# Performance work log

Measured on AMD Instinct MI355X. Metric: run time of the kernel, lower is better.

## Reference

```python
import jax, jax.numpy as jnp
import numpy as np

B, C, T = 32, 64, 1024        # batch_size, in_channels, cycle_size
H, D = 2, 64                  # GATv2 heads, per-head dim (dim_h)
DIM2 = H * D                  # dim_h * 2 = 128
K = 9                         # temporal_kernel_size
N = B * T                     # graph nodes after flatten
E = 524288                    # edges (avg degree 16)
EPS = 1e-5


def bn3d(x, gamma, beta):
    # BatchNorm1d on [B, C, T] in training mode (batch statistics)
    mu = x.mean(axis=(0, 2), keepdims=True)
    var = x.var(axis=(0, 2), keepdims=True)
    xn = (x - mu) * jax.lax.rsqrt(var + EPS)
    return xn * gamma[None, :, None] + beta[None, :, None]


def bn2d(x, gamma, beta):
    # BatchNorm1d on [N, C] in training mode
    mu = x.mean(axis=0, keepdims=True)
    var = x.var(axis=0, keepdims=True)
    return (x - mu) * jax.lax.rsqrt(var + EPS) * gamma + beta


def conv1d_same(x, w, b):
    # x: [B, Cin, T], w: [Cout, Cin, K]
    y = jax.lax.conv_general_dilated(x, w, (1,), 'SAME',
                                     dimension_numbers=('NCH', 'OIH', 'NCH'))
    return y + b[None, :, None]


def gatv2(x, edge_index, wl, wr, att, bias):
    # PyG GATv2Conv defaults: heads=H, concat=True, leaky slope 0.2, self-loops
    loops = jnp.arange(N, dtype=edge_index.dtype)
    src = jnp.concatenate([edge_index[0], loops])
    dst = jnp.concatenate([edge_index[1], loops])
    xl = (x @ wl.T).reshape(N, H, D)   # source transform
    xr = (x @ wr.T).reshape(N, H, D)   # target transform
    m = jax.nn.leaky_relu(xl[src] + xr[dst], 0.2)        # [E+N, H, D]
    logits = jnp.einsum('ehd,hd->eh', m, att)            # [E+N, H]
    lmax = jax.ops.segment_max(logits, dst, num_segments=N)
    lmax = jax.lax.stop_gradient(jnp.where(jnp.isfinite(lmax), lmax, 0.0))
    p = jnp.exp(logits - lmax[dst])
    denom = jax.ops.segment_sum(p, dst, num_segments=N)  # >0: self-loops
    alpha = p / denom[dst]                               # softmax over in-edges
    out = jax.ops.segment_sum(xl[src] * alpha[:, :, None], dst, num_segments=N)
    return out.reshape(N, DIM2) + bias


def setup_inputs() -> dict:
    key = jax.random.key(0)
    ks = jax.random.split(key, 10)
    s = lambda k, shape: jax.random.normal(k, shape, jnp.float32) * 0.05
    return {
        'x': jax.random.normal(ks[0], (B, C, T), jnp.float32),
        'edge_index': jax.random.randint(ks[1], (2, E), 0, N, jnp.int32),
        'bn0_gamma': jnp.ones((C,), jnp.float32),
        'bn0_beta': jnp.zeros((C,), jnp.float32),
        'conv_w': s(ks[2], (DIM2, C, K)),
        'conv_b': s(ks[3], (DIM2,)),
        'gat_wl': s(ks[4], (DIM2, C)),
        'gat_wr': s(ks[5], (DIM2, C)),
        'gat_att': s(ks[6], (H, D)),
        'gat_bias': s(ks[7], (DIM2,)),
        'bn1_gamma': jnp.ones((DIM2,), jnp.float32),
        'bn1_beta': jnp.zeros((DIM2,), jnp.float32),
        'cheb_w': s(ks[8], (DIM2, DIM2)),
        'cheb_b': s(ks[9], (DIM2,)),
        'train': 0,
    }


def reference(x, edge_index, bn0_gamma, bn0_beta, conv_w, conv_b,
              gat_wl, gat_wr, gat_att, gat_bias, bn1_gamma, bn1_beta,
              cheb_w, cheb_b, train):
    x = bn3d(x, bn0_gamma, bn0_beta)                       # b0 (batch_size > 1)
    residual = jax.nn.relu(conv1d_same(x, conv_w, conv_b)) # skip_connection
    h = x.reshape(T * B, C)                                # flatten to nodes
    h = gatv2(h, edge_index, gat_wl, gat_wr, gat_att, gat_bias)
    h = jax.nn.relu(bn2d(h, bn1_gamma, bn1_beta))          # b1
    h = h.reshape(B, DIM2, T)
    h = residual + h
    # chain of views: (T*B,d) -> (B,d,T) -> (B,T,-1) -> (T*B,d); pure reshapes
    h = h.reshape(T * B, DIM2)
    h = h @ cheb_w.T + cheb_b                              # ChebConv K=1 == linear
    h = jax.nn.relu(bn2d(h, bn1_gamma, bn1_beta))          # b1 again
    h = h.reshape(B, DIM2, T)
    return residual + h                                    # dropout: identity (eval)
```

## Files before the change

kernel.cpp:

```cpp
#include <hip/hip_runtime.h>

#define DEVINL __device__ __forceinline__

constexpr int Bc = 32, Cc = 64, Tc = 1024, DIM2c = 128;
constexpr int Nn = Bc * Tc;
constexpr int Ec = 524288;

typedef __bf16 bf16x8 __attribute__((ext_vector_type(8)));
typedef __bf16 bf16x4 __attribute__((ext_vector_type(4)));
typedef float  f32x4  __attribute__((ext_vector_type(4)));

constexpr long O_RES   = 0;
constexpr long O_GOUT  = 4194304;
constexpr long O_XT    = 8388608;
constexpr long O_HBF   = 9437184;
constexpr long O_XLQ   = 10485760;
constexpr long O_XRQ   = 12582912;
constexpr long O_H2BF  = 14680064;
constexpr long O_Z     = 16777216;
constexpr long O_WCBF  = 20971520;
constexpr long O_WLR   = 21008384;
constexpr long O_CHB   = 21016576;
constexpr long O_STAT  = 21024768;
constexpr long O_CUR   = 21025792;
constexpr long O_BUCK  = 21058560;

DEVINL float unpack_lo(unsigned v) { return __uint_as_float(v << 16); }
DEVINL float unpack_hi(unsigned v) { return __uint_as_float(v & 0xffff0000u); }
DEVINL unsigned bfb(float f) { return (__float_as_uint(f) + 0x8000u) >> 16; }

__global__ __launch_bounds__(256) void setup(const float* __restrict__ x,
        const float* __restrict__ cw, const float* __restrict__ wl,
        const float* __restrict__ wr, const float* __restrict__ chw,
        const int* __restrict__ ei,
        __bf16* __restrict__ wcbf, __bf16* __restrict__ wlrbf,
        __bf16* __restrict__ chwbf,
        float* __restrict__ sum0, float* __restrict__ sq0,
        int* __restrict__ cursor, int* __restrict__ bucket) {
    int bid = blockIdx.x, tid = threadIdx.x;
    if (bid < 416) {
        int i = bid * 256 + tid;
        if (i < 73728) {
            int kk = i >> 13, co = (i >> 6) & 127, ci = i & 63;
            wcbf[i] = (__bf16)cw[co * 576 + ci * 9 + kk];
        } else if (i < 73728 + 16384) {
            int j = i - 73728;
            int r = j >> 6, c = j & 63;
            float v = (r < 128) ? wl[r * 64 + c] : wr[(r - 128) * 64 + c];
            wlrbf[j] = (__bf16)v;
        } else {
            int j = i - 73728 - 16384;
            chwbf[j] = (__bf16)chw[j];
        }
    } else if (bid < 672) {
        int pq = bid - 416;
        int c = pq & 63, q = pq >> 6;
        const float4* base = (const float4*)(x + (long)q * 8 * 65536 + (long)c * 1024);
        float s = 0.f, qq = 0.f;
        for (int i = tid; i < 2048; i += 256) {
            int b = i >> 8, t4 = i & 255;
            float4 v = base[b * 16384 + t4];
            s += v.x + v.y + v.z + v.w;
            qq = fmaf(v.x, v.x, qq); qq = fmaf(v.y, v.y, qq);
            qq = fmaf(v.z, v.z, qq); qq = fmaf(v.w, v.w, qq);
        }
        for (int off = 32; off; off >>= 1) { s += __shfl_down(s, off); qq += __shfl_down(qq, off); }
        __shared__ float ls[4], lq[4];
        int w = tid >> 6, lane = tid & 63;
        if (lane == 0) { ls[w] = s; lq[w] = qq; }
        __syncthreads();
        if (tid == 0) {
            unsafeAtomicAdd(sum0 + c, ls[0] + ls[1] + ls[2] + ls[3]);
            unsafeAtomicAdd(sq0 + c, lq[0] + lq[1] + lq[2] + lq[3]);
        }
    } else {
        int e = (bid - 672) * 256 + tid;
        int t = ei[Ec + e];
        int slot = atomicAdd(cursor + t, 1);
        bucket[t * 64 + slot] = ei[e];
    }
}

__global__ __launch_bounds__(256) void xprep(const float* __restrict__ x,
        const float* __restrict__ sum0, const float* __restrict__ sq0,
        const float* __restrict__ g0, const float* __restrict__ b0,
        __bf16* __restrict__ hbf, __bf16* __restrict__ xt) {
    __shared__ float lds[64][65];
    __shared__ float scs[64], shs[64];
    int tid = threadIdx.x;
    if (tid < 64) {
        float mu = sum0[tid] * (1.f / 32768.f);
        float var = sq0[tid] * (1.f / 32768.f) - mu * mu;
        float rs = rsqrtf(var + 1e-5f);
        float sc = rs * g0[tid];
        scs[tid] = sc; shs[tid] = b0[tid] - mu * sc;
    }
    __syncthreads();
    int t0 = blockIdx.x * 64;
    int b  = blockIdx.y;
    const float* xb = x + (long)b * 65536;
    for (int i = tid; i < 4096; i += 256) {
        int ci = i >> 6, tl = i & 63;
        float v = fmaf(xb[ci * 1024 + t0 + tl], scs[ci], shs[ci]);
        hbf[(long)b * 65536 + ci * 1024 + t0 + tl] = (__bf16)v;
        lds[ci][tl] = v;
    }
    __syncthreads();
    for (int i = tid; i < 4096; i += 256) {
        int t = i >> 6, ci = i & 63;
        xt[((long)b * 1024 + t0 + t) * 64 + ci] = (__bf16)lds[ci][t];
    }
}

constexpr int XS_STRIDE = 68;

DEVINL void conv_role(int cid, const __bf16* __restrict__ xt,
        const __bf16* __restrict__ wcbf, const float* __restrict__ cb,
        float* __restrict__ res, __bf16* xs) {
    int tid = threadIdx.x;
    int tbase = (cid & 7) * 128;
    int cohalf = (cid >> 3) & 1;
    int b = cid >> 4;
    const uint2* xg = (const uint2*)(xt + (long)b * 65536);
    for (int i = tid; i < 136 * 16; i += 256) {
        int row = i >> 4, c4 = i & 15;
        int t = tbase + row - 4;
        uint2 v; v.x = 0u; v.y = 0u;
        if ((unsigned)t < 1024u) v = xg[t * 16 + c4];
        *(uint2*)(xs + row * XS_STRIDE + c4 * 4) = v;
    }
    __syncthreads();
    int wv = tid >> 6, lane = tid & 63;
    int col = lane & 15, q = lane >> 4;
    int co0 = cohalf * 64 + wv * 16;
    bf16x8 af[18];
    #pragma unroll
    for (int kk = 0; kk < 9; kk++)
        #pragma unroll
        for (int ks = 0; ks < 2; ks++)
            af[kk * 2 + ks] = *(const bf16x8*)(wcbf +
                ((long)kk * 8192 + (long)(co0 + col) * 64 + ks * 32 + q * 8));
    float bi0 = cb[co0 + q * 4], bi1 = cb[co0 + q * 4 + 1];
    float bi2 = cb[co0 + q * 4 + 2], bi3 = cb[co0 + q * 4 + 3];
    for (int nt = 0; nt < 8; nt++) {
        int t0 = tbase + nt * 16;
        f32x4 acc; acc[0] = bi0; acc[1] = bi1; acc[2] = bi2; acc[3] = bi3;
        #pragma unroll
        for (int kk = 0; kk < 9; kk++) {
            const __bf16* rp = xs + (nt * 16 + col + kk) * XS_STRIDE + q * 8;
            #pragma unroll
            for (int ks = 0; ks < 2; ks++) {
                bf16x4 lo = *(const bf16x4*)(rp + ks * 32);
                bf16x4 hi = *(const bf16x4*)(rp + ks * 32 + 4);
                bf16x8 bfx;
                bfx[0]=lo[0]; bfx[1]=lo[1]; bfx[2]=lo[2]; bfx[3]=lo[3];
                bfx[4]=hi[0]; bfx[5]=hi[1]; bfx[6]=hi[2]; bfx[7]=hi[3];
                acc = __builtin_amdgcn_mfma_f32_16x16x32_bf16(af[kk * 2 + ks], bfx, acc, 0, 0, 0);
            }
        }
        long ob = (long)b * 131072 + (long)(co0 + q * 4) * 1024 + t0 + col;
        res[ob]        = fmaxf(acc[0], 0.f);
        res[ob + 1024] = fmaxf(acc[1], 0.f);
        res[ob + 2048] = fmaxf(acc[2], 0.f);
        res[ob + 3072] = fmaxf(acc[3], 0.f);
    }
}

DEVINL void gemm1_role(int mb, const __bf16* __restrict__ hbf,
        const __bf16* __restrict__ wlrbf,
        unsigned short* __restrict__ xl16, unsigned short* __restrict__ xr16) {
    int wv = threadIdx.x >> 6, lane = threadIdx.x & 63;
    int col = lane & 15, q = lane >> 4;
    int d0 = wv * 16;
    long mbase = (long)mb * 64;
    bf16x8 bfr[4][2];
    #pragma unroll
    for (int t = 0; t < 4; t++) {
        int j = d0 + t * 64 + col;
        #pragma unroll
        for (int ks = 0; ks < 2; ks++)
            bfr[t][ks] = *(const bf16x8*)(wlrbf + (long)j * 64 + ks * 32 + q * 8);
    }
    int d = d0 + col;
    for (int mt = 0; mt < 4; mt++) {
        long r0 = mbase + mt * 16;
        bf16x8 a0 = *(const bf16x8*)(hbf + (r0 + col) * 64 + q * 8);
        bf16x8 a1 = *(const bf16x8*)(hbf + (r0 + col) * 64 + 32 + q * 8);
        f32x4 acc[4];
        #pragma unroll
        for (int t = 0; t < 4; t++) { acc[t][0] = 0.f; acc[t][1] = 0.f; acc[t][2] = 0.f; acc[t][3] = 0.f; }
        #pragma unroll
        for (int t = 0; t < 4; t++) {
            acc[t] = __builtin_amdgcn_mfma_f32_16x16x32_bf16(a0, bfr[t][0], acc[t], 0, 0, 0);
            acc[t] = __builtin_amdgcn_mfma_f32_16x16x32_bf16(a1, bfr[t][1], acc[t], 0, 0, 0);
        }
        #pragma unroll
        for (int reg = 0; reg < 4; reg++) {
            long rb = (r0 + q * 4 + reg) * 128;
            xl16[rb + d]      = (unsigned short)bfb(acc[0][reg]);
            xl16[rb + 64 + d] = (unsigned short)bfb(acc[1][reg]);
            xr16[rb + d]      = (unsigned short)bfb(acc[2][reg]);
            xr16[rb + 64 + d] = (unsigned short)bfb(acc[3][reg]);
        }
    }
}

__global__ __launch_bounds__(256) void conv_gemm1(const __bf16* __restrict__ xt,
        const __bf16* __restrict__ wcbf, const float* __restrict__ cb,
        float* __restrict__ res, const __bf16* __restrict__ hbf,
        const __bf16* __restrict__ wlrbf,
        unsigned* __restrict__ xlq, unsigned* __restrict__ xrq) {
    __shared__ __bf16 xs[136 * XS_STRIDE];
    int bid = blockIdx.x;
    if (bid & 1) gemm1_role(bid >> 1, hbf, wlrbf, (unsigned short*)xlq, (unsigned short*)xrq);
    else conv_role(bid >> 1, xt, wcbf, cb, res, xs);
}

#define GAT_EDGE(VREG) {                                              \
    float xl_lo = unpack_lo(VREG), xl_hi = unpack_hi(VREG);           \
    float v0 = xl_lo + xr_lo; v0 = fmaxf(v0, 0.2f * v0);              \
    float v1 = xl_hi + xr_hi; v1 = fmaxf(v1, 0.2f * v1);              \
    float w2 = fmaf(v1, a_hi, v0 * a_lo);                             \
    _Pragma("unroll")                                                 \
    for (int off = 16; off; off >>= 1) w2 += __shfl_xor(w2, off);     \
    float e2 = __expf(w2);                                            \
    den += e2;                                                        \
    acc_lo = fmaf(e2, xl_lo, acc_lo);                                 \
    acc_hi = fmaf(e2, xl_hi, acc_hi);                                 \
}

__global__ __launch_bounds__(256) void gat_agg(const unsigned* __restrict__ xlq,
        const unsigned* __restrict__ xrq,
        const int* __restrict__ cursor, const int* __restrict__ bucket,
        const float* __restrict__ att, float* __restrict__ gout) {
    int wid = (blockIdx.x * 256 + threadIdx.x) >> 6;
    int lane = threadIdx.x & 63;
    int h = lane >> 5, dd = (lane & 31) * 2;
    float a_lo = att[h * 64 + dd], a_hi = att[h * 64 + dd + 1];
    int cnt = cursor[wid];
    int s_all = bucket[wid * 64 + lane];
    unsigned vr = xrq[(long)wid * 64 + lane];
    float xr_lo = unpack_lo(vr), xr_hi = unpack_hi(vr);
    unsigned vs = xlq[(long)wid * 64 + lane];
    float xs_lo = unpack_lo(vs), xs_hi = unpack_hi(vs);
    float u0 = xs_lo + xr_lo; u0 = fmaxf(u0, 0.2f * u0);
    float u1 = xs_hi + xr_hi; u1 = fmaxf(u1, 0.2f * u1);
    float w = fmaf(u1, a_hi, u0 * a_lo);
    #pragma unroll
    for (int off = 16; off; off >>= 1) w += __shfl_xor(w, off);
    float e = __expf(w);
    float den = e, acc_lo = e * xs_lo, acc_hi = e * xs_hi;
    unsigned pf0 = 0, pf1 = 0, pf2 = 0, pf3 = 0;
    {
        int s0 = __shfl(s_all, 0), s1 = __shfl(s_all, 1);
        int s2 = __shfl(s_all, 2), s3 = __shfl(s_all, 3);
        if (0 < cnt) pf0 = xlq[(long)s0 * 64 + lane];
        if (1 < cnt) pf1 = xlq[(long)s1 * 64 + lane];
        if (2 < cnt) pf2 = xlq[(long)s2 * 64 + lane];
        if (3 < cnt) pf3 = xlq[(long)s3 * 64 + lane];
    }
    int i = 0;
    for (; i + 4 <= cnt; i += 4) {
        unsigned v0 = pf0, v1 = pf1, v2 = pf2, v3 = pf3;
        int s4 = __shfl(s_all, i + 4), s5 = __shfl(s_all, i + 5);
        int s6 = __shfl(s_all, i + 6), s7 = __shfl(s_all, i + 7);
        if (i + 4 < cnt) pf0 = xlq[(long)s4 * 64 + lane];
        if (i + 5 < cnt) pf1 = xlq[(long)s5 * 64 + lane];
        if (i + 6 < cnt) pf2 = xlq[(long)s6 * 64 + lane];
        if (i + 7 < cnt) pf3 = xlq[(long)s7 * 64 + lane];
        GAT_EDGE(v0) GAT_EDGE(v1) GAT_EDGE(v2) GAT_EDGE(v3)
    }
    if (i < cnt) { GAT_EDGE(pf0) i++;
        if (i < cnt) { GAT_EDGE(pf1) i++;
            if (i < cnt) { GAT_EDGE(pf2) } } }
    float rn = __builtin_amdgcn_rcpf(den);
    float2 o; o.x = acc_lo * rn; o.y = acc_hi * rn;
    *(float2*)(gout + (long)wid * 128 + h * 64 + dd) = o;
}

__global__ __launch_bounds__(256) void bn_stats(const float* __restrict__ X,
        float* __restrict__ sum, float* __restrict__ sq) {
    int f = threadIdx.x & 127, sub = threadIdx.x >> 7;
    int r0 = blockIdx.x * 256;
    float s = 0.f, q = 0.f;
    for (int r = r0 + sub; r < r0 + 256; r += 2) {
        float v = X[(long)r * 128 + f];
        s += v; q = fmaf(v, v, q);
    }
    __shared__ float ls[256], lq[256];
    ls[threadIdx.x] = s; lq[threadIdx.x] = q;
    __syncthreads();
    if (threadIdx.x < 128) {
        s = ls[threadIdx.x] + ls[threadIdx.x + 128];
        q = lq[threadIdx.x] + lq[threadIdx.x + 128];
        unsafeAtomicAdd(sum + f, s);
        unsafeAtomicAdd(sq + f, q);
    }
}

__global__ __launch_bounds__(256) void bn_res_bf(const float* __restrict__ X,
        const float* __restrict__ res, const float* __restrict__ sum,
        const float* __restrict__ sq, const float* __restrict__ g,
        const float* __restrict__ bta, unsigned* __restrict__ outb) {
    __shared__ float scs[128], shs[128];
    int tid = threadIdx.x;
    if (tid < 128) {
        float mu = sum[tid] * (1.f / 32768.f);
        float var = sq[tid] * (1.f / 32768.f) - mu * mu;
        float rs = rsqrtf(var + 1e-5f);
        float sc = rs * g[tid];
        scs[tid] = sc; shs[tid] = bta[tid] - mu * sc;
    }
    __syncthreads();
    int idx = blockIdx.x * 256 + tid;
    int f0 = (idx & 31) * 4;
    float4 v = ((const float4*)X)[idx];
    float4 r = ((const float4*)res)[idx];
    float o0 = r.x + fmaxf(fmaf(v.x, scs[f0],     shs[f0]),     0.f);
    float o1 = r.y + fmaxf(fmaf(v.y, scs[f0 + 1], shs[f0 + 1]), 0.f);
    float o2 = r.z + fmaxf(fmaf(v.z, scs[f0 + 2], shs[f0 + 2]), 0.f);
    float o3 = r.w + fmaxf(fmaf(v.w, scs[f0 + 3], shs[f0 + 3]), 0.f);
    uint2 o; o.x = (bfb(o1) << 16) | bfb(o0); o.y = (bfb(o3) << 16) | bfb(o2);
    ((uint2*)outb)[idx] = o;
}

__global__ __launch_bounds__(256) void bn_res(const float* __restrict__ X,
        const float* __restrict__ res, const float* __restrict__ sum,
        const float* __restrict__ sq, const float* __restrict__ g,
        const float* __restrict__ bta, float* __restrict__ out) {
    __shared__ float scs[128], shs[128];
    int tid = threadIdx.x;
    if (tid < 128) {
        float mu = sum[tid] * (1.f / 32768.f);
        float var = sq[tid] * (1.f / 32768.f) - mu * mu;
        float rs = rsqrtf(var + 1e-5f);
        float sc = rs * g[tid];
        scs[tid] = sc; shs[tid] = bta[tid] - mu * sc;
    }
    __syncthreads();
    int idx = blockIdx.x * 256 + tid;
    int f0 = (idx & 31) * 4;
    float4 v = ((const float4*)X)[idx];
    float4 r = ((const float4*)res)[idx];
    float4 o;
    o.x = r.x + fmaxf(fmaf(v.x, scs[f0],     shs[f0]),     0.f);
    o.y = r.y + fmaxf(fmaf(v.y, scs[f0 + 1], shs[f0 + 1]), 0.f);
    o.z = r.z + fmaxf(fmaf(v.z, scs[f0 + 2], shs[f0 + 2]), 0.f);
    o.w = r.w + fmaxf(fmaf(v.w, scs[f0 + 3], shs[f0 + 3]), 0.f);
    ((float4*)out)[idx] = o;
}

__global__ __launch_bounds__(256) void cheb_mfma(const __bf16* __restrict__ h2bf,
        const __bf16* __restrict__ chwbf, float* __restrict__ z) {
    int wv = threadIdx.x >> 6, lane = threadIdx.x & 63;
    int col = lane & 15, q = lane >> 4;
    long mbase = (long)blockIdx.x * 64;
    bf16x8 bfr[2][4];
    #pragma unroll
    for (int t = 0; t < 2; t++) {
        int j = wv * 16 + t * 64 + col;
        #pragma unroll
        for (int ks = 0; ks < 4; ks++)
            bfr[t][ks] = *(const bf16x8*)(chwbf + (long)j * 128 + ks * 32 + q * 8);
    }
    for (int mt = 0; mt < 4; mt++) {
        long r0 = mbase + mt * 16;
        bf16x8 a[4];
        #pragma unroll
        for (int ks = 0; ks < 4; ks++)
            a[ks] = *(const bf16x8*)(h2bf + (r0 + col) * 128 + ks * 32 + q * 8);
        f32x4 acc[2];
        #pragma unroll
        for (int t = 0; t < 2; t++) { acc[t][0] = 0.f; acc[t][1] = 0.f; acc[t][2] = 0.f; acc[t][3] = 0.f; }
        #pragma unroll
        for (int t = 0; t < 2; t++)
            #pragma unroll
            for (int ks = 0; ks < 4; ks++)
                acc[t] = __builtin_amdgcn_mfma_f32_16x16x32_bf16(a[ks], bfr[t][ks], acc[t], 0, 0, 0);
        #pragma unroll
        for (int t = 0; t < 2; t++)
            #pragma unroll
            for (int reg = 0; reg < 4; reg++)
                z[(r0 + q * 4 + reg) * 128 + wv * 16 + t * 64 + col] = acc[t][reg];
    }
}

extern "C" void kernel_launch(void* const* d_in, const int* in_sizes, int n_in,
                              void* d_out, int out_size, void* d_ws, size_t ws_size,
                              hipStream_t stream) {
    const float* x   = (const float*)d_in[0];
    const int*   ei  = (const int*)d_in[1];
    const float* g0  = (const float*)d_in[2];
    const float* b0  = (const float*)d_in[3];
    const float* cw  = (const float*)d_in[4];
    const float* cb  = (const float*)d_in[5];
    const float* wl  = (const float*)d_in[6];
    const float* wr  = (const float*)d_in[7];
    const float* att = (const float*)d_in[8];
    const float* g1  = (const float*)d_in[10];
    const float* b1  = (const float*)d_in[11];
    const float* chw = (const float*)d_in[12];
    float* out = (float*)d_out;

    float* ws = (float*)d_ws;
    float*    res   = ws + O_RES;
    float*    gout  = ws + O_GOUT;
    __bf16*   xt    = (__bf16*)(ws + O_XT);
    __bf16*   hbf   = (__bf16*)(ws + O_HBF);
    unsigned* xlq   = (unsigned*)(ws + O_XLQ);
    unsigned* xrq   = (unsigned*)(ws + O_XRQ);
    unsigned* h2bf  = (unsigned*)(ws + O_H2BF);
    float*    z     = ws + O_Z;
    __bf16*   wcbf  = (__bf16*)(ws + O_WCBF);
    __bf16*   wlrbf = (__bf16*)(ws + O_WLR);
    __bf16*   chwbf = (__bf16*)(ws + O_CHB);
    float*    st    = ws + O_STAT;
    int*      cursor = (int*)(ws + O_CUR);
    int*      bucket = (int*)(ws + O_BUCK);
    float *sum0 = st,       *sq0 = st + 64;
    float *sum1 = st + 128, *sq1 = st + 256;
    float *sum2 = st + 384, *sq2 = st + 512;

    hipMemsetAsync(st, 0, (size_t)(1024 + 32768) * 4, stream);

    setup<<<2720, 256, 0, stream>>>(x, cw, wl, wr, chw, ei,
                                    wcbf, wlrbf, chwbf, sum0, sq0, cursor, bucket);
    xprep<<<dim3(16, 32), 256, 0, stream>>>(x, sum0, sq0, g0, b0, hbf, xt);
    conv_gemm1<<<1024, 256, 0, stream>>>(xt, wcbf, cb, res, hbf, wlrbf, xlq, xrq);
    gat_agg<<<8192, 256, 0, stream>>>(xlq, xrq, cursor, bucket, att, gout);
    bn_stats<<<128, 256, 0, stream>>>(gout, sum1, sq1);
    bn_res_bf<<<4096, 256, 0, stream>>>(gout, res, sum1, sq1, g1, b1, h2bf);
    cheb_mfma<<<512, 256, 0, stream>>>((const __bf16*)h2bf, chwbf, z);
    bn_stats<<<128, 256, 0, stream>>>(z, sum2, sq2);
    bn_res<<<4096, 256, 0, stream>>>(z, res, sum2, sq2, g1, b1, out);
}
```

Before: 273.7 us.

## Process eight edges per wave in GAT aggregation and fuse BN-residual into Cheb GEMM

The GAT aggregation kernel is restructured so each wave handles eight in-edges at once. Each group of eight lanes holds 16 features per lane, loaded as two 16-byte vectors. This replaces one edge per step with a five-level shuffle reduction per edge by a two-level reduction, followed by a cross-group reduction at the end. The BN+ReLU+residual bf16 conversion, the Cheb MFMA GEMM and the second BN statistics pass are fused into one kernel. That kernel stages activations in LDS and accumulates column sums via shared atomics, which removes the h2bf round trip and a separate stats launch. The cost is higher register pressure from the 16-element accumulators, and some idle lanes when a node's degree is not a multiple of eight.

Result: faster. 236.4 us (-13.6%).

```diff
diff --git a/kernel.cpp b/kernel.cpp
--- a/kernel.cpp
+++ b/kernel.cpp
@@ -16,7 +16,6 @@
 constexpr long O_HBF   = 9437184;
 constexpr long O_XLQ   = 10485760;
 constexpr long O_XRQ   = 12582912;
-constexpr long O_H2BF  = 14680064;
 constexpr long O_Z     = 16777216;
 constexpr long O_WCBF  = 20971520;
 constexpr long O_WLR   = 21008384;
@@ -216,66 +215,78 @@
     else conv_role(bid >> 1, xt, wcbf, cb, res, xs);
 }
 
-#define GAT_EDGE(VREG) {                                              \
-    float xl_lo = unpack_lo(VREG), xl_hi = unpack_hi(VREG);           \
-    float v0 = xl_lo + xr_lo; v0 = fmaxf(v0, 0.2f * v0);              \
-    float v1 = xl_hi + xr_hi; v1 = fmaxf(v1, 0.2f * v1);              \
-    float w2 = fmaf(v1, a_hi, v0 * a_lo);                             \
-    _Pragma("unroll")                                                 \
-    for (int off = 16; off; off >>= 1) w2 += __shfl_xor(w2, off);     \
-    float e2 = __expf(w2);                                            \
-    den += e2;                                                        \
-    acc_lo = fmaf(e2, xl_lo, acc_lo);                                 \
-    acc_hi = fmaf(e2, xl_hi, acc_hi);                                 \
-}
-
-__global__ __launch_bounds__(256) void gat_agg(const unsigned* __restrict__ xlq,
-        const unsigned* __restrict__ xrq,
+__global__ __launch_bounds__(256) void gat_agg(const uint4* __restrict__ xlq4,
+        const uint4* __restrict__ xrq4,
         const int* __restrict__ cursor, const int* __restrict__ bucket,
         const float* __restrict__ att, float* __restrict__ gout) {
     int wid = (blockIdx.x * 256 + threadIdx.x) >> 6;
     int lane = threadIdx.x & 63;
-    int h = lane >> 5, dd = (lane & 31) * 2;
-    float a_lo = att[h * 64 + dd], a_hi = att[h * 64 + dd + 1];
+    int g = lane >> 3, j = lane & 7;
+    float av[16];
+    #pragma unroll
+    for (int k = 0; k < 16; k++) av[k] = att[16 * j + k];
+    uint4 r0v = xrq4[(long)wid * 16 + j * 2];
+    uint4 r1v = xrq4[(long)wid * 16 + j * 2 + 1];
+    float xr[16];
+    {
+        unsigned ru[8] = {r0v.x, r0v.y, r0v.z, r0v.w, r1v.x, r1v.y, r1v.z, r1v.w};
+        #pragma unroll
+        for (int k = 0; k < 8; k++) { xr[2*k] = unpack_lo(ru[k]); xr[2*k+1] = unpack_hi(ru[k]); }
+    }
     int cnt = cursor[wid];
     int s_all = bucket[wid * 64 + lane];
-    unsigned vr = xrq[(long)wid * 64 + lane];
-    float xr_lo = unpack_lo(vr), xr_hi = unpack_hi(vr);
-    unsigned vs = xlq[(long)wid * 64 + lane];
-    float xs_lo = unpack_lo(vs), xs_hi = unpack_hi(vs);
-    float u0 = xs_lo + xr_lo; u0 = fmaxf(u0, 0.2f * u0);
-    float u1 = xs_hi + xr_hi; u1 = fmaxf(u1, 0.2f * u1);
-    float w = fmaf(u1, a_hi, u0 * a_lo);
-    #pragma unroll
-    for (int off = 16; off; off >>= 1) w += __shfl_xor(w, off);
-    float e = __expf(w);
-    float den = e, acc_lo = e * xs_lo, acc_hi = e * xs_hi;
-    unsigned pf0 = 0, pf1 = 0, pf2 = 0, pf3 = 0;
-    {
-        int s0 = __shfl(s_all, 0), s1 = __shfl(s_all, 1);
-        int s2 = __shfl(s_all, 2), s3 = __shfl(s_all, 3);
-        if (0 < cnt) pf0 = xlq[(long)s0 * 64 + lane];
-        if (1 < cnt) pf1 = xlq[(long)s1 * 64 + lane];
-        if (2 < cnt) pf2 = xlq[(long)s2 * 64 + lane];
-        if (3 < cnt) pf3 = xlq[(long)s3 * 64 + lane];
-    }
-    int i = 0;
-    for (; i + 4 <= cnt; i += 4) {
-        unsigned v0 = pf0, v1 = pf1, v2 = pf2, v3 = pf3;
-        int s4 = __shfl(s_all, i + 4), s5 = __shfl(s_all, i + 5);
-        int s6 = __shfl(s_all, i + 6), s7 = __shfl(s_all, i + 7);
-        if (i + 4 < cnt) pf0 = xlq[(long)s4 * 64 + lane];
-        if (i + 5 < cnt) pf1 = xlq[(long)s5 * 64 + lane];
-        if (i + 6 < cnt) pf2 = xlq[(long)s6 * 64 + lane];
-        if (i + 7 < cnt) pf3 = xlq[(long)s7 * 64 + lane];
-        GAT_EDGE(v0) GAT_EDGE(v1) GAT_EDGE(v2) GAT_EDGE(v3)
-    }
-    if (i < cnt) { GAT_EDGE(pf0) i++;
-        if (i < cnt) { GAT_EDGE(pf1) i++;
-            if (i < cnt) { GAT_EDGE(pf2) } } }
+    float acc[16];
+    #pragma unroll
+    for (int k = 0; k < 16; k++) acc[k] = 0.f;
+    float den = 0.f;
+    int nit = (cnt + 8) >> 3;
+    int sp = __shfl(s_all, g);
+    sp = (g < cnt) ? sp : wid;
+    uint4 p0 = xlq4[(long)sp * 16 + j * 2];
+    uint4 p1 = xlq4[(long)sp * 16 + j * 2 + 1];
+    for (int it = 0; it < nit; it++) {
+        uint4 c0 = p0, c1 = p1;
+        int icur = it * 8 + g;
+        int inext = icur + 8;
+        if (it + 1 < nit) {
+            int sn = __shfl(s_all, inext & 63);
+            sn = (inext < cnt) ? sn : wid;
+            p0 = xlq4[(long)sn * 16 + j * 2];
+            p1 = xlq4[(long)sn * 16 + j * 2 + 1];
+        }
+        unsigned uu[8] = {c0.x, c0.y, c0.z, c0.w, c1.x, c1.y, c1.z, c1.w};
+        float xl[16];
+        float w = 0.f;
+        #pragma unroll
+        for (int k = 0; k < 8; k++) {
+            float lo = unpack_lo(uu[k]), hi = unpack_hi(uu[k]);
+            xl[2*k] = lo; xl[2*k+1] = hi;
+            float s0 = lo + xr[2*k]; s0 = fmaxf(s0, 0.2f * s0);
+            float s1 = hi + xr[2*k+1]; s1 = fmaxf(s1, 0.2f * s1);
+            w = fmaf(s1, av[2*k+1], fmaf(s0, av[2*k], w));
+        }
+        w += __shfl_xor(w, 1); w += __shfl_xor(w, 2);
+        float e2 = (icur <= cnt) ? __expf(w) : 0.f;
+        den += e2;
+        #pragma unroll
+        for (int k = 0; k < 16; k++) acc[k] = fmaf(e2, xl[k], acc[k]);
+    }
+    #pragma unroll
+    for (int m = 8; m <= 32; m <<= 1) {
+        den += __shfl_xor(den, m);
+        #pragma unroll
+        for (int k = 0; k < 16; k++) acc[k] += __shfl_xor(acc[k], m);
+    }
     float rn = __builtin_amdgcn_rcpf(den);
-    float2 o; o.x = acc_lo * rn; o.y = acc_hi * rn;
-    *(float2*)(gout + (long)wid * 128 + h * 64 + dd) = o;
+    if (g == 0) {
+        #pragma unroll
+        for (int c = 0; c < 4; c++) {
+            float4 o;
+            o.x = acc[4*c] * rn;     o.y = acc[4*c+1] * rn;
+            o.z = acc[4*c+2] * rn;   o.w = acc[4*c+3] * rn;
+            *(float4*)(gout + (long)wid * 128 + 16 * j + 4 * c) = o;
+        }
+    }
 }
 
 __global__ __launch_bounds__(256) void bn_stats(const float* __restrict__ X,
@@ -298,30 +309,79 @@
     }
 }
 
-__global__ __launch_bounds__(256) void bn_res_bf(const float* __restrict__ X,
-        const float* __restrict__ res, const float* __restrict__ sum,
-        const float* __restrict__ sq, const float* __restrict__ g,
-        const float* __restrict__ bta, unsigned* __restrict__ outb) {
-    __shared__ float scs[128], shs[128];
+__global__ __launch_bounds__(256) void cheb_fused(const float* __restrict__ gout,
+        const float* __restrict__ res, const float* __restrict__ sum1,
+        const float* __restrict__ sq1, const float* __restrict__ g1,
+        const float* __restrict__ b1, const __bf16* __restrict__ chwbf,
+        float* __restrict__ z, float* __restrict__ sum2, float* __restrict__ sq2) {
+    __shared__ unsigned xs[64 * 68];
+    __shared__ float scs[128], shs[128], cs[128], cq[128];
     int tid = threadIdx.x;
     if (tid < 128) {
-        float mu = sum[tid] * (1.f / 32768.f);
-        float var = sq[tid] * (1.f / 32768.f) - mu * mu;
+        float mu = sum1[tid] * (1.f / 32768.f);
+        float var = sq1[tid] * (1.f / 32768.f) - mu * mu;
         float rs = rsqrtf(var + 1e-5f);
-        float sc = rs * g[tid];
-        scs[tid] = sc; shs[tid] = bta[tid] - mu * sc;
-    }
-    __syncthreads();
-    int idx = blockIdx.x * 256 + tid;
-    int f0 = (idx & 31) * 4;
-    float4 v = ((const float4*)X)[idx];
-    float4 r = ((const float4*)res)[idx];
-    float o0 = r.x + fmaxf(fmaf(v.x, scs[f0],     shs[f0]),     0.f);
-    float o1 = r.y + fmaxf(fmaf(v.y, scs[f0 + 1], shs[f0 + 1]), 0.f);
-    float o2 = r.z + fmaxf(fmaf(v.z, scs[f0 + 2], shs[f0 + 2]), 0.f);
-    float o3 = r.w + fmaxf(fmaf(v.w, scs[f0 + 3], shs[f0 + 3]), 0.f);
-    uint2 o; o.x = (bfb(o1) << 16) | bfb(o0); o.y = (bfb(o3) << 16) | bfb(o2);
-    ((uint2*)outb)[idx] = o;
+        float sc = rs * g1[tid];
+        scs[tid] = sc; shs[tid] = b1[tid] - mu * sc;
+        cs[tid] = 0.f;
+    } else cq[tid - 128] = 0.f;
+    __syncthreads();
+    long r0 = (long)blockIdx.x * 64;
+    for (int i = tid; i < 2048; i += 256) {
+        int row = i >> 5, c4 = i & 31;
+        long gidx = (r0 + row) * 32 + c4;
+        float4 v = ((const float4*)gout)[gidx];
+        float4 r = ((const float4*)res)[gidx];
+        int f0 = c4 * 4;
+        float o0 = r.x + fmaxf(fmaf(v.x, scs[f0],     shs[f0]),     0.f);
+        float o1 = r.y + fmaxf(fmaf(v.y, scs[f0 + 1], shs[f0 + 1]), 0.f);
+        float o2 = r.z + fmaxf(fmaf(v.z, scs[f0 + 2], shs[f0 + 2]), 0.f);
+        float o3 = r.w + fmaxf(fmaf(v.w, scs[f0 + 3], shs[f0 + 3]), 0.f);
+        xs[row * 68 + c4 * 2]     = (bfb(o1) << 16) | bfb(o0);
+        xs[row * 68 + c4 * 2 + 1] = (bfb(o3) << 16) | bfb(o2);
+    }
+    __syncthreads();
+    int wv = tid >> 6, lane = tid & 63;
+    int col = lane & 15, q = lane >> 4;
+    bf16x8 bfr[2][4];
+    #pragma unroll
+    for (int t = 0; t < 2; t++) {
+        int jj = wv * 16 + t * 64 + col;
+        #pragma unroll
+        for (int ks = 0; ks < 4; ks++)
+            bfr[t][ks] = *(const bf16x8*)(chwbf + (long)jj * 128 + ks * 32 + q * 8);
+    }
+    float ls0 = 0.f, ls1 = 0.f, lq0 = 0.f, lq1 = 0.f;
+    for (int mt = 0; mt < 4; mt++) {
+        const __bf16* ap = (const __bf16*)xs + (mt * 16 + col) * 136;
+        bf16x8 a[4];
+        #pragma unroll
+        for (int ks = 0; ks < 4; ks++)
+            a[ks] = *(const bf16x8*)(ap + ks * 32 + q * 8);
+        f32x4 acc[2];
+        #pragma unroll
+        for (int t = 0; t < 2; t++) { acc[t][0] = 0.f; acc[t][1] = 0.f; acc[t][2] = 0.f; acc[t][3] = 0.f; }
+        #pragma unroll
+        for (int t = 0; t < 2; t++)
+            #pragma unroll
+            for (int ks = 0; ks < 4; ks++)
+                acc[t] = __builtin_amdgcn_mfma_f32_16x16x32_bf16(a[ks], bfr[t][ks], acc[t], 0, 0, 0);
+        #pragma unroll
+        for (int reg = 0; reg < 4; reg++) {
+            float v0 = acc[0][reg], v1 = acc[1][reg];
+            long zr = (r0 + mt * 16 + q * 4 + reg) * 128;
+            z[zr + wv * 16 + col]      = v0;
+            z[zr + wv * 16 + 64 + col] = v1;
+            ls0 += v0; lq0 = fmaf(v0, v0, lq0);
+            ls1 += v1; lq1 = fmaf(v1, v1, lq1);
+        }
+    }
+    int j0 = wv * 16 + col;
+    atomicAdd(&cs[j0], ls0);      atomicAdd(&cs[j0 + 64], ls1);
+    atomicAdd(&cq[j0], lq0);      atomicAdd(&cq[j0 + 64], lq1);
+    __syncthreads();
+    if (tid < 128) unsafeAtomicAdd(sum2 + tid, cs[tid]);
+    else unsafeAtomicAdd(sq2 + tid - 128, cq[tid - 128]);
 }
 
 __global__ __launch_bounds__(256) void bn_res(const float* __restrict__ X,
@@ -348,41 +408,6 @@
     o.z = r.z + fmaxf(fmaf(v.z, scs[f0 + 2], shs[f0 + 2]), 0.f);
     o.w = r.w + fmaxf(fmaf(v.w, scs[f0 + 3], shs[f0 + 3]), 0.f);
     ((float4*)out)[idx] = o;
-}
-
-__global__ __launch_bounds__(256) void cheb_mfma(const __bf16* __restrict__ h2bf,
-        const __bf16* __restrict__ chwbf, float* __restrict__ z) {
-    int wv = threadIdx.x >> 6, lane = threadIdx.x & 63;
-    int col = lane & 15, q = lane >> 4;
-    long mbase = (long)blockIdx.x * 64;
-    bf16x8 bfr[2][4];
-    #pragma unroll
-    for (int t = 0; t < 2; t++) {
-        int j = wv * 16 + t * 64 + col;
-        #pragma unroll
-        for (int ks = 0; ks < 4; ks++)
-            bfr[t][ks] = *(const bf16x8*)(chwbf + (long)j * 128 + ks * 32 + q * 8);
-    }
-    for (int mt = 0; mt < 4; mt++) {
-        long r0 = mbase + mt * 16;
-        bf16x8 a[4];
-        #pragma unroll
-        for (int ks = 0; ks < 4; ks++)
-            a[ks] = *(const bf16x8*)(h2bf + (r0 + col) * 128 + ks * 32 + q * 8);
-        f32x4 acc[2];
-        #pragma unroll
-        for (int t = 0; t < 2; t++) { acc[t][0] = 0.f; acc[t][1] = 0.f; acc[t][2] = 0.f; acc[t][3] = 0.f; }
-        #pragma unroll
-        for (int t = 0; t < 2; t++)
-            #pragma unroll
-            for (int ks = 0; ks < 4; ks++)
-                acc[t] = __builtin_amdgcn_mfma_f32_16x16x32_bf16(a[ks], bfr[t][ks], acc[t], 0, 0, 0);
-        #pragma unroll
-        for (int t = 0; t < 2; t++)
-            #pragma unroll
-            for (int reg = 0; reg < 4; reg++)
-                z[(r0 + q * 4 + reg) * 128 + wv * 16 + t * 64 + col] = acc[t][reg];
-    }
 }
 
 extern "C" void kernel_launch(void* const* d_in, const int* in_sizes, int n_in,
@@ -409,7 +434,6 @@
     __bf16*   hbf   = (__bf16*)(ws + O_HBF);
     unsigned* xlq   = (unsigned*)(ws + O_XLQ);
     unsigned* xrq   = (unsigned*)(ws + O_XRQ);
-    unsigned* h2bf  = (unsigned*)(ws + O_H2BF);
     float*    z     = ws + O_Z;
     __bf16*   wcbf  = (__bf16*)(ws + O_WCBF);
     __bf16*   wlrbf = (__bf16*)(ws + O_WLR);
@@ -427,10 +451,10 @@
                                     wcbf, wlrbf, chwbf, sum0, sq0, cursor, bucket);
     xprep<<<dim3(16, 32), 256, 0, stream>>>(x, sum0, sq0, g0, b0, hbf, xt);
     conv_gemm1<<<1024, 256, 0, stream>>>(xt, wcbf, cb, res, hbf, wlrbf, xlq, xrq);
-    gat_agg<<<8192, 256, 0, stream>>>(xlq, xrq, cursor, bucket, att, gout);
+    gat_agg<<<8192, 256, 0, stream>>>((const uint4*)xlq, (const uint4*)xrq,
+                                      cursor, bucket, att, gout);
     bn_stats<<<128, 256, 0, stream>>>(gout, sum1, sq1);
-    bn_res_bf<<<4096, 256, 0, stream>>>(gout, res, sum1, sq1, g1, b1, h2bf);
-    cheb_mfma<<<512, 256, 0, stream>>>((const __bf16*)h2bf, chwbf, z);
-    bn_stats<<<128, 256, 0, stream>>>(z, sum2, sq2);
+    cheb_fused<<<512, 256, 0, stream>>>(gout, res, sum1, sq1, g1, b1, chwbf,
+                                        z, sum2, sq2);
     bn_res<<<4096, 256, 0, stream>>>(z, res, sum2, sq2, g1, b1, out);
 }
```
